# Performance work log

Measured on AMD Instinct MI355X. Metric: run time of the kernel, lower is better.

The kernel has to match this reference:

```python
import jax, jax.numpy as jnp
import numpy as np

N_NODES = 150000
D = 64
N_EDGES = 2000000  # bidirectional: 2 * num_train_edges


def setup_inputs() -> dict:
    key = jax.random.key(0)
    k1, k2, k3, k4, k5 = jax.random.split(key, 5)
    nodes_emb = jax.random.normal(k1, (N_NODES, D), dtype=jnp.float32)
    src = jax.random.randint(k2, (N_EDGES,), 0, N_NODES, dtype=jnp.int64 if jax.config.jax_enable_x64 else jnp.int32).astype(jnp.int32)
    dst = jax.random.randint(k3, (N_EDGES,), 0, N_NODES, dtype=jnp.int32)
    W1 = jax.random.normal(k4, (2 * D, D), dtype=jnp.float32) * (1.0 / np.sqrt(2 * D))
    b1 = jnp.zeros((D,), dtype=jnp.float32)
    W2 = jax.random.normal(k5, (D, 1), dtype=jnp.float32) * (1.0 / np.sqrt(D))
    b2 = jnp.zeros((1,), dtype=jnp.float32)
    return {"nodes_emb": nodes_emb, "src": src, "dst": dst,
            "W1": W1, "b1": b1, "W2": W2, "b2": b2}


def reference(nodes_emb, src, dst, W1, b1, W2, b2):
    # Gather per-edge endpoint embeddings and concat: [E, 2D]
    emb_src = nodes_emb[src]          # [E, D]
    emb_dst = nodes_emb[dst]          # [E, D]
    edge_emb = jnp.concatenate([emb_src, emb_dst], axis=1)  # [E, 2D]
    # 2-layer MLP edge scorer: Linear(2D->D) -> ReLU -> Linear(D->1)
    h = jax.nn.relu(edge_emb @ W1 + b1)  # [E, D]
    edge_logits = h @ W2 + b2            # [E, 1]
    return edge_logits
```

## Files before the change

kernel.cpp:

```cpp
#include <hip/hip_runtime.h>

typedef __attribute__((ext_vector_type(8))) short bf16x8;
typedef __attribute__((ext_vector_type(4))) float f32x4;
typedef __attribute__((ext_vector_type(2))) unsigned int u32x2;
typedef __attribute__((ext_vector_type(4))) unsigned int u32x4;

#define LDSTR 136
#define TPW 8

static __device__ __forceinline__ unsigned int pack2bf(float x, float y) {
  unsigned int ux = __builtin_bit_cast(unsigned int, x);
  ux += 0x7fffu + ((ux >> 16) & 1u);
  unsigned int uy = __builtin_bit_cast(unsigned int, y);
  uy += 0x7fffu + ((uy >> 16) & 1u);
  return (ux >> 16) | (uy & 0xffff0000u);
}
static __device__ __forceinline__ unsigned short f2bf_s(float x) {
  unsigned int ux = __builtin_bit_cast(unsigned int, x);
  ux += 0x7fffu + ((ux >> 16) & 1u);
  return (unsigned short)(ux >> 16);
}
static __device__ __forceinline__ bf16x8 make_afrag(float4 lo, float4 hi) {
  u32x4 p;
  p[0] = pack2bf(lo.x, lo.y);
  p[1] = pack2bf(lo.z, lo.w);
  p[2] = pack2bf(hi.x, hi.y);
  p[3] = pack2bf(hi.z, hi.w);
  return __builtin_bit_cast(bf16x8, p);
}

__global__ __launch_bounds__(256) void node_proj(
    const float* __restrict__ emb,
    const float* __restrict__ W1,
    u32x2* __restrict__ P,
    u32x2* __restrict__ Q,
    int N, int ntiles)
{
  __shared__ unsigned short ls_w1t[64 * LDSTR];
  const int tid  = threadIdx.x;
  const int wave = tid >> 6;
  const int lane = tid & 63;
  const int l15  = lane & 15;
  const int quad = lane >> 4;

  for (int i = tid; i < 64 * 128; i += 256) {
    int k = i >> 6, n = i & 63;
    ls_w1t[n * LDSTR + k] = f2bf_s(W1[i]);
  }
  __syncthreads();

  bf16x8 bfragP[4][2], bfragQ[4][2];
  #pragma unroll
  for (int tn = 0; tn < 4; ++tn)
    #pragma unroll
    for (int s = 0; s < 2; ++s) {
      bfragP[tn][s] = *(const bf16x8*)&ls_w1t[(tn * 16 + l15) * LDSTR + s * 32 + quad * 8];
      bfragQ[tn][s] = *(const bf16x8*)&ls_w1t[(tn * 16 + l15) * LDSTR + 64 + s * 32 + quad * 8];
    }

  for (int tile = blockIdx.x * 4 + wave; tile < ntiles; tile += gridDim.x * 4) {
    const int base = tile * 16;

    bf16x8 afr0, afr1;
    {
      int node = base + l15;
      node = (node < N) ? node : N - 1;
      const float* rp = emb + (long long)node * 64 + quad * 8;
      afr0 = make_afrag(*(const float4*)(rp),      *(const float4*)(rp + 4));
      afr1 = make_afrag(*(const float4*)(rp + 32), *(const float4*)(rp + 36));
    }

    f32x4 aP[4], aQ[4];
    #pragma unroll
    for (int tn = 0; tn < 4; ++tn) { aP[tn] = (f32x4){0,0,0,0}; aQ[tn] = (f32x4){0,0,0,0}; }
    #pragma unroll
    for (int tn = 0; tn < 4; ++tn) {
      aP[tn] = __builtin_amdgcn_mfma_f32_16x16x32_bf16(afr0, bfragP[tn][0], aP[tn], 0, 0, 0);
      aQ[tn] = __builtin_amdgcn_mfma_f32_16x16x32_bf16(afr0, bfragQ[tn][0], aQ[tn], 0, 0, 0);
      aP[tn] = __builtin_amdgcn_mfma_f32_16x16x32_bf16(afr1, bfragP[tn][1], aP[tn], 0, 0, 0);
      aQ[tn] = __builtin_amdgcn_mfma_f32_16x16x32_bf16(afr1, bfragQ[tn][1], aQ[tn], 0, 0, 0);
    }

    #pragma unroll
    for (int r = 0; r < 4; ++r) {
      const int m = base + quad * 4 + r;
      if (m < N) {
        u32x2 vp, vq;
        vp[0] = pack2bf(aP[0][r], aP[1][r]);
        vp[1] = pack2bf(aP[2][r], aP[3][r]);
        vq[0] = pack2bf(aQ[0][r], aQ[1][r]);
        vq[1] = pack2bf(aQ[2][r], aQ[3][r]);
        P[(long long)m * 16 + l15] = vp;
        Q[(long long)m * 16 + l15] = vq;
      }
    }
  }
}

__global__ __launch_bounds__(256) void edge_score(
    const unsigned short* __restrict__ P,
    const unsigned short* __restrict__ Q,
    const int*   __restrict__ src,
    const int*   __restrict__ dst,
    const float* __restrict__ b1,
    const float* __restrict__ W2,
    const float* __restrict__ b2,
    float*       __restrict__ out,
    int E)
{
  const int tid  = blockIdx.x * 256 + threadIdx.x;
  const int lane = threadIdx.x & 63;
  const int s    = lane & 7;
  const int g    = lane >> 3;
  const int wid  = tid >> 6;
  const int nwav = gridDim.x * 4;

  float b1v[8], w2v[8];
  #pragma unroll
  for (int j = 0; j < 8; ++j) {
    const int pos = s * 8 + j;
    const int ch  = (pos & 3) * 16 + (pos >> 2);
    b1v[j] = b1[ch];
    w2v[j] = W2[ch];
  }
  const float b2v = b2[0];
  const int so16 = s * 8;

#define DOT8(PV, QV, ACC)                                                     \
  {                                                                           \
    u32x4 pu = __builtin_bit_cast(u32x4, PV);                                 \
    u32x4 qu = __builtin_bit_cast(u32x4, QV);                                 \
    _Pragma("unroll")                                                         \
    for (int i = 0; i < 4; ++i) {                                             \
      float pl = __builtin_bit_cast(float, pu[i] << 16);                      \
      float ph = __builtin_bit_cast(float, pu[i] & 0xffff0000u);              \
      float ql = __builtin_bit_cast(float, qu[i] << 16);                      \
      float qh = __builtin_bit_cast(float, qu[i] & 0xffff0000u);              \
      float h0 = fmaxf(pl + ql + b1v[2 * i], 0.f);                            \
      float h1 = fmaxf(ph + qh + b1v[2 * i + 1], 0.f);                        \
      ACC = __builtin_fmaf(h0, w2v[2 * i], ACC);                              \
      ACC = __builtin_fmaf(h1, w2v[2 * i + 1], ACC);                          \
    }                                                                         \
  }

  const int step = nwav * 16;
  for (int e0 = wid * 16; e0 < E; e0 += step) {
    int eA = e0 + g;
    int eB = e0 + 8 + g;
    const int eAc = (eA < E) ? eA : (E - 1);
    const int eBc = (eB < E) ? eB : (E - 1);
    const int siA = src[eAc], diA = dst[eAc];
    const int siB = src[eBc], diB = dst[eBc];

    const bf16x8 pvA = *(const bf16x8*)(P + (long long)siA * 64 + so16);
    const bf16x8 qvA = *(const bf16x8*)(Q + (long long)diA * 64 + so16);
    const bf16x8 pvB = *(const bf16x8*)(P + (long long)siB * 64 + so16);
    const bf16x8 qvB = *(const bf16x8*)(Q + (long long)diB * 64 + so16);

    float accA = 0.f, accB = 0.f;
    DOT8(pvA, qvA, accA);
    DOT8(pvB, qvB, accB);

    accA += __shfl_xor(accA, 1); accB += __shfl_xor(accB, 1);
    accA += __shfl_xor(accA, 2); accB += __shfl_xor(accB, 2);
    accA += __shfl_xor(accA, 4); accB += __shfl_xor(accB, 4);

    if (s == 0) {
      if (eA < E) out[eA] = accA + b2v;
      if (eB < E) out[eB] = accB + b2v;
    }
  }
#undef DOT8
}

__global__ __launch_bounds__(256) void edge_mlp_f32(
    const float* __restrict__ nodes_emb, const int* __restrict__ src,
    const int* __restrict__ dst, const float* __restrict__ W1,
    const float* __restrict__ b1, const float* __restrict__ W2,
    const float* __restrict__ b2, float* __restrict__ out, int E)
{
  __shared__ unsigned short ls_w1t[64 * LDSTR];
  __shared__ float ls_b1[64];
  __shared__ float ls_w2[64];
  const int tid = threadIdx.x, wave = tid >> 6, lane = tid & 63;
  const int l15 = lane & 15, quad = lane >> 4;
  for (int i = tid; i < 64 * 128; i += 256) {
    int n = i >> 7, k = i & 127;
    ls_w1t[n * LDSTR + k] = f2bf_s(W1[k * 64 + n]);
  }
  if (tid < 64) { ls_b1[tid] = b1[tid]; ls_w2[tid] = W2[tid]; }
  __syncthreads();
  bf16x8 bfrag[4][4];
  #pragma unroll
  for (int tn = 0; tn < 4; ++tn)
    #pragma unroll
    for (int s = 0; s < 4; ++s)
      bfrag[tn][s] = *(const bf16x8*)&ls_w1t[(tn * 16 + l15) * LDSTR + s * 32 + quad * 8];
  float myb1[4], myw2[4];
  #pragma unroll
  for (int tn = 0; tn < 4; ++tn) { myb1[tn] = ls_b1[tn*16+l15]; myw2[tn] = ls_w2[tn*16+l15]; }
  const float b2v = b2[0];
  const int wave_base = blockIdx.x * (TPW * 64) + wave * (TPW * 16);
  #pragma unroll 1
  for (int t = 0; t < TPW; ++t) {
    const int tile_base = wave_base + t * 16;
    if (tile_base >= E) break;
    const int e = tile_base + l15;
    const int si = src[e], di = dst[e];
    const float* srow = nodes_emb + (long long)si * 64 + quad * 8;
    const float* drow = nodes_emb + (long long)di * 64 + quad * 8;
    float4 v0 = *(const float4*)(srow),      v1 = *(const float4*)(srow + 4);
    float4 v2 = *(const float4*)(srow + 32), v3 = *(const float4*)(srow + 36);
    float4 v4 = *(const float4*)(drow),      v5 = *(const float4*)(drow + 4);
    float4 v6 = *(const float4*)(drow + 32), v7 = *(const float4*)(drow + 36);
    bf16x8 afr[4] = {make_afrag(v0,v1), make_afrag(v2,v3), make_afrag(v4,v5), make_afrag(v6,v7)};
    f32x4 acc[4];
    #pragma unroll
    for (int tn = 0; tn < 4; ++tn) acc[tn] = (f32x4){0.f,0.f,0.f,0.f};
    #pragma unroll
    for (int s = 0; s < 4; ++s)
      #pragma unroll
      for (int tn = 0; tn < 4; ++tn)
        acc[tn] = __builtin_amdgcn_mfma_f32_16x16x32_bf16(afr[s], bfrag[tn][s], acc[tn], 0, 0, 0);
    #pragma unroll
    for (int r = 0; r < 4; ++r) {
      float p = 0.f;
      #pragma unroll
      for (int tn = 0; tn < 4; ++tn) {
        float h = fmaxf(acc[tn][r] + myb1[tn], 0.f);
        p = __builtin_fmaf(h, myw2[tn], p);
      }
      p += __shfl_xor(p, 1); p += __shfl_xor(p, 2);
      p += __shfl_xor(p, 4); p += __shfl_xor(p, 8);
      if (l15 == 0) out[tile_base + quad * 4 + r] = p + b2v;
    }
  }
}

extern "C" void kernel_launch(void* const* d_in, const int* in_sizes, int n_in,
                              void* d_out, int out_size, void* d_ws, size_t ws_size,
                              hipStream_t stream) {
  const float* nodes_emb = (const float*)d_in[0];
  const int*   src       = (const int*)d_in[1];
  const int*   dst       = (const int*)d_in[2];
  const float* W1        = (const float*)d_in[3];
  const float* b1        = (const float*)d_in[4];
  const float* W2        = (const float*)d_in[5];
  const float* b2        = (const float*)d_in[6];
  float* out = (float*)d_out;

  const int E = in_sizes[1];
  const int nodes_elems = in_sizes[0];
  const int N = nodes_elems / 64;
  const size_t szP = (size_t)nodes_elems * 2;
  const size_t need = szP * 2;

  if (ws_size >= need) {
    u32x2* P = (u32x2*)d_ws;
    u32x2* Q = (u32x2*)((char*)d_ws + szP);
    const int ntiles = (N + 15) / 16;
    hipLaunchKernelGGL(node_proj, dim3(512), dim3(256), 0, stream,
                       nodes_emb, W1, P, Q, N, ntiles);
    hipLaunchKernelGGL(edge_score, dim3(2048), dim3(256), 0, stream,
                       (const unsigned short*)P, (const unsigned short*)Q,
                       src, dst, b1, W2, b2, out, E);
  } else {
    const int epb = TPW * 64;
    const int blocks = (E + epb - 1) / epb;
    hipLaunchKernelGGL(edge_mlp_f32, dim3(blocks), dim3(256), 0, stream,
                       nodes_emb, src, dst, W1, b1, W2, b2, out, E);
  }
}
```

Measured before the change: 173.6 us.

## Fold b1 into node projection and software-pipeline index loads in edge scorer

Adds the first-layer bias to the Q projection in node_proj, so the edge kernel no longer adds b1 per element. The edge kernel now handles 32 edges per wave-iteration instead of 16. It prefetches the next iteration's src/dst indices while the current gathers are in flight, which hides index-load latency behind the dependent gathers. This costs more registers, and rounding the biased Q values to bf16 slightly changes numerics. It also switches gather address arithmetic to 32-bit int indexing.

```diff
diff --git a/kernel.cpp b/kernel.cpp
--- a/kernel.cpp
+++ b/kernel.cpp
@@ -32,6 +32,7 @@
 __global__ __launch_bounds__(256) void node_proj(
     const float* __restrict__ emb,
     const float* __restrict__ W1,
+    const float* __restrict__ b1,
     u32x2* __restrict__ P,
     u32x2* __restrict__ Q,
     int N, int ntiles)
@@ -49,6 +50,10 @@
   }
   __syncthreads();
 
+  float b1q[4];
+  #pragma unroll
+  for (int tn = 0; tn < 4; ++tn) b1q[tn] = b1[tn * 16 + l15];
+
   bf16x8 bfragP[4][2], bfragQ[4][2];
   #pragma unroll
   for (int tn = 0; tn < 4; ++tn)
@@ -88,8 +93,8 @@
         u32x2 vp, vq;
         vp[0] = pack2bf(aP[0][r], aP[1][r]);
         vp[1] = pack2bf(aP[2][r], aP[3][r]);
-        vq[0] = pack2bf(aQ[0][r], aQ[1][r]);
-        vq[1] = pack2bf(aQ[2][r], aQ[3][r]);
+        vq[0] = pack2bf(aQ[0][r] + b1q[0], aQ[1][r] + b1q[1]);
+        vq[1] = pack2bf(aQ[2][r] + b1q[2], aQ[3][r] + b1q[3]);
         P[(long long)m * 16 + l15] = vp;
         Q[(long long)m * 16 + l15] = vq;
       }
@@ -102,7 +107,6 @@
     const unsigned short* __restrict__ Q,
     const int*   __restrict__ src,
     const int*   __restrict__ dst,
-    const float* __restrict__ b1,
     const float* __restrict__ W2,
     const float* __restrict__ b2,
     float*       __restrict__ out,
@@ -113,18 +117,17 @@
   const int s    = lane & 7;
   const int g    = lane >> 3;
   const int wid  = tid >> 6;
-  const int nwav = gridDim.x * 4;
-
-  float b1v[8], w2v[8];
+  const int step = gridDim.x * 4 * 32;
+
+  float w2v[8];
   #pragma unroll
   for (int j = 0; j < 8; ++j) {
     const int pos = s * 8 + j;
     const int ch  = (pos & 3) * 16 + (pos >> 2);
-    b1v[j] = b1[ch];
     w2v[j] = W2[ch];
   }
   const float b2v = b2[0];
-  const int so16 = s * 8;
+  const int so = s * 8;
 
 #define DOT8(PV, QV, ACC)                                                     \
   {                                                                           \
@@ -136,39 +139,77 @@
       float ph = __builtin_bit_cast(float, pu[i] & 0xffff0000u);              \
       float ql = __builtin_bit_cast(float, qu[i] << 16);                      \
       float qh = __builtin_bit_cast(float, qu[i] & 0xffff0000u);              \
-      float h0 = fmaxf(pl + ql + b1v[2 * i], 0.f);                            \
-      float h1 = fmaxf(ph + qh + b1v[2 * i + 1], 0.f);                        \
+      float h0 = fmaxf(pl + ql, 0.f);                                         \
+      float h1 = fmaxf(ph + qh, 0.f);                                         \
       ACC = __builtin_fmaf(h0, w2v[2 * i], ACC);                              \
       ACC = __builtin_fmaf(h1, w2v[2 * i + 1], ACC);                          \
     }                                                                         \
   }
 
-  const int step = nwav * 16;
-  for (int e0 = wid * 16; e0 < E; e0 += step) {
-    int eA = e0 + g;
-    int eB = e0 + 8 + g;
-    const int eAc = (eA < E) ? eA : (E - 1);
-    const int eBc = (eB < E) ? eB : (E - 1);
-    const int siA = src[eAc], diA = dst[eAc];
-    const int siB = src[eBc], diB = dst[eBc];
-
-    const bf16x8 pvA = *(const bf16x8*)(P + (long long)siA * 64 + so16);
-    const bf16x8 qvA = *(const bf16x8*)(Q + (long long)diA * 64 + so16);
-    const bf16x8 pvB = *(const bf16x8*)(P + (long long)siB * 64 + so16);
-    const bf16x8 qvB = *(const bf16x8*)(Q + (long long)diB * 64 + so16);
-
-    float accA = 0.f, accB = 0.f;
-    DOT8(pvA, qvA, accA);
-    DOT8(pvB, qvB, accB);
+  int e0 = wid * 32;
+  if (e0 >= E) return;
+
+  int iA, iB, iC, iD, jA, jB, jC, jD;
+  {
+    const int eA = e0 + g,      eAc = (eA < E) ? eA : E - 1;
+    const int eB = e0 + 8 + g,  eBc = (eB < E) ? eB : E - 1;
+    const int eC = e0 + 16 + g, eCc = (eC < E) ? eC : E - 1;
+    const int eD = e0 + 24 + g, eDc = (eD < E) ? eD : E - 1;
+    iA = src[eAc]; jA = dst[eAc];
+    iB = src[eBc]; jB = dst[eBc];
+    iC = src[eCc]; jC = dst[eCc];
+    iD = src[eDc]; jD = dst[eDc];
+  }
+
+  while (true) {
+    const bf16x8 pA = *(const bf16x8*)(P + iA * 64 + so);
+    const bf16x8 qA = *(const bf16x8*)(Q + jA * 64 + so);
+    const bf16x8 pB = *(const bf16x8*)(P + iB * 64 + so);
+    const bf16x8 qB = *(const bf16x8*)(Q + jB * 64 + so);
+    const bf16x8 pC = *(const bf16x8*)(P + iC * 64 + so);
+    const bf16x8 qC = *(const bf16x8*)(Q + jC * 64 + so);
+    const bf16x8 pD = *(const bf16x8*)(P + iD * 64 + so);
+    const bf16x8 qD = *(const bf16x8*)(Q + jD * 64 + so);
+
+    const int en = e0 + step;
+    const bool more = (en < E);
+    if (more) {
+      const int fA = en + g,      fAc = (fA < E) ? fA : E - 1;
+      const int fB = en + 8 + g,  fBc = (fB < E) ? fB : E - 1;
+      const int fC = en + 16 + g, fCc = (fC < E) ? fC : E - 1;
+      const int fD = en + 24 + g, fDc = (fD < E) ? fD : E - 1;
+      iA = src[fAc]; jA = dst[fAc];
+      iB = src[fBc]; jB = dst[fBc];
+      iC = src[fCc]; jC = dst[fCc];
+      iD = src[fDc]; jD = dst[fDc];
+    }
+
+    float accA = 0.f, accB = 0.f, accC = 0.f, accD = 0.f;
+    DOT8(pA, qA, accA);
+    DOT8(pB, qB, accB);
+    DOT8(pC, qC, accC);
+    DOT8(pD, qD, accD);
 
     accA += __shfl_xor(accA, 1); accB += __shfl_xor(accB, 1);
+    accC += __shfl_xor(accC, 1); accD += __shfl_xor(accD, 1);
     accA += __shfl_xor(accA, 2); accB += __shfl_xor(accB, 2);
+    accC += __shfl_xor(accC, 2); accD += __shfl_xor(accD, 2);
     accA += __shfl_xor(accA, 4); accB += __shfl_xor(accB, 4);
+    accC += __shfl_xor(accC, 4); accD += __shfl_xor(accD, 4);
 
     if (s == 0) {
+      const int eA = e0 + g;
+      const int eB = e0 + 8 + g;
+      const int eC = e0 + 16 + g;
+      const int eD = e0 + 24 + g;
       if (eA < E) out[eA] = accA + b2v;
       if (eB < E) out[eB] = accB + b2v;
-    }
+      if (eC < E) out[eC] = accC + b2v;
+      if (eD < E) out[eD] = accD + b2v;
+    }
+
+    if (!more) break;
+    e0 = en;
   }
 #undef DOT8
 }
@@ -260,10 +301,10 @@
     u32x2* Q = (u32x2*)((char*)d_ws + szP);
     const int ntiles = (N + 15) / 16;
     hipLaunchKernelGGL(node_proj, dim3(512), dim3(256), 0, stream,
-                       nodes_emb, W1, P, Q, N, ntiles);
+                       nodes_emb, W1, b1, P, Q, N, ntiles);
     hipLaunchKernelGGL(edge_score, dim3(2048), dim3(256), 0, stream,
                        (const unsigned short*)P, (const unsigned short*)Q,
-                       src, dst, b1, W2, b2, out, E);
+                       src, dst, W2, b2, out, E);
   } else {
     const int epb = TPW * 64;
     const int blocks = (E + epb - 1) / epb;
```

After: 172.6 us. About the same (-0.6%).
